# Performance work log

Measured on AMD Instinct MI355X. Metric: run time of the kernel, lower is better.

## Reference

```python
import jax, jax.numpy as jnp
import numpy as np

B, T, C = 1024, 512, 41


def setup_inputs() -> dict:
    key = jax.random.key(0)
    k1, k2, k3, k4 = jax.random.split(key, 4)
    x = jax.random.normal(k1, (B, T, C), dtype=jnp.float32)
    # torchcrf initializes all transition params uniform(-0.1, 0.1)
    start_transitions = jax.random.uniform(k2, (C,), minval=-0.1, maxval=0.1, dtype=jnp.float32)
    end_transitions = jax.random.uniform(k3, (C,), minval=-0.1, maxval=0.1, dtype=jnp.float32)
    transitions = jax.random.uniform(k4, (C, C), minval=-0.1, maxval=0.1, dtype=jnp.float32)
    return {"x": x, "start_transitions": start_transitions,
            "end_transitions": end_transitions, "transitions": transitions}


def reference(x, start_transitions, end_transitions, transitions):
    # Viterbi decode (torchcrf CRF.decode, batch_first, no mask -> full length)
    # x: [B, T, C] emissions
    score0 = start_transitions[None, :] + x[:, 0]  # [B, C]

    def step(score, emit_t):
        # score: [B, C] best score ending in each tag at time t
        # emit_t: [B, C] emissions at time t+1
        cand = score[:, :, None] + transitions[None, :, :] + emit_t[:, None, :]  # [B, Cprev, Cnext]
        best = jnp.max(cand, axis=1)      # [B, C]
        bp = jnp.argmax(cand, axis=1)     # [B, C] backpointer: best previous tag
        return best, bp

    emits = jnp.swapaxes(x[:, 1:], 0, 1)  # [T-1, B, C]
    final, bps = jax.lax.scan(step, score0, emits)
    final = final + end_transitions[None, :]  # [B, C]
    last_tag = jnp.argmax(final, axis=1)      # [B] tag at time T-1

    def back(tag, bp_t):
        # tag: [B] tag at time t+1; bp_t: [B, C] backpointers into time t
        prev = jnp.take_along_axis(bp_t, tag[:, None], axis=1)[:, 0]
        return prev, tag

    first_tag, tags_rest = jax.lax.scan(back, last_tag, bps, reverse=True)
    # tags_rest[t] is the tag at time t+1 (t = 0..T-2); first_tag is tag at time 0
    tags = jnp.concatenate([first_tag[:, None], jnp.swapaxes(tags_rest, 0, 1)], axis=1)  # [B, T]
    return tags.astype(jnp.int64)
```

## Files before the change

kernel.cpp:

```cpp
#include <hip/hip_runtime.h>

#define BB 1024
#define TT 512
#define CC 41
#define BPS 64

__device__ __forceinline__ float rlanef(float xv, int l) {
    return __int_as_float(__builtin_amdgcn_readlane(__float_as_int(xv), l));
}

__global__ __launch_bounds__(64) void crf_viterbi_kernel(
    const float* __restrict__ x,
    const float* __restrict__ start_t,
    const float* __restrict__ end_t,
    const float* __restrict__ trans,
    int* __restrict__ out)
{
    __shared__ unsigned char bp_lds[(TT - 1) * BPS];
    __shared__ int tags_lds[TT];

    const int lane = threadIdx.x;
    const int c = (lane < CC) ? lane : (CC - 1);

    float trans_reg[CC];
    #pragma unroll
    for (int p = 0; p < CC; ++p) trans_reg[p] = trans[p * CC + c];

    const float* xb = x + (size_t)blockIdx.x * TT * CC;

    float myscore = start_t[c] + xb[c];

    float emit_cur = xb[1 * CC + c];
    float emit_nxt = xb[2 * CC + c];

    for (int t = 1; t < TT; ++t) {
        const int tf = (t + 2 < TT) ? (t + 2) : (TT - 1);
        const float emit_fut = xb[(size_t)tf * CC + c];

        float sp[CC];
        #pragma unroll
        for (int p = 0; p < CC; ++p) sp[p] = rlanef(myscore, p);

        float v[CC];
        int  ix[CC];
        #pragma unroll
        for (int p = 0; p < CC; ++p) {
            v[p]  = (sp[p] + trans_reg[p]) + emit_cur;
            ix[p] = p;
        }

#define COMBINE(i, j) do { \
            if (v[(j)] > v[(i)]) { v[(i)] = v[(j)]; ix[(i)] = ix[(j)]; } \
        } while (0)
        #pragma unroll
        for (int i = 0; i < 20; ++i) COMBINE(2 * i, 2 * i + 1);
        #pragma unroll
        for (int i = 0; i < 10; ++i) COMBINE(4 * i, 4 * i + 2);
        #pragma unroll
        for (int i = 0; i < 5; ++i)  COMBINE(8 * i, 8 * i + 4);
        COMBINE(0, 8);
        COMBINE(16, 24);
        COMBINE(0, 16);
        COMBINE(32, 40);
        COMBINE(0, 32);
#undef COMBINE

        myscore = v[0];
        bp_lds[(t - 1) * BPS + lane] = (unsigned char)ix[0];

        emit_cur = emit_nxt;
        emit_nxt = emit_fut;
    }

    const float fin = myscore + end_t[c];

    float bestv = rlanef(fin, 0);
    int tag = 0;
    #pragma unroll
    for (int i = 1; i < CC; ++i) {
        const float vi = rlanef(fin, i);
        if (vi > bestv) { bestv = vi; tag = i; }
    }

    __syncthreads();

    if (lane == 0) tags_lds[TT - 1] = tag;
    for (int g = 31; g >= 0; --g) {
        const int base = g * 16;
        unsigned int rowv[16];
        #pragma unroll
        for (int j = 0; j < 16; ++j)
            rowv[j] = (unsigned int)bp_lds[(base + j) * BPS + lane];
        #pragma unroll
        for (int j = 15; j >= 0; --j) {
            const int r = base + j;
            if (r < TT - 1) {
                tag = (int)__builtin_amdgcn_readlane((int)rowv[j], tag);
                if (lane == 0) tags_lds[r] = tag;
            }
        }
    }
    __syncthreads();

    int* ob = out + (size_t)blockIdx.x * TT;
    #pragma unroll
    for (int i = 0; i < TT / 64; ++i) ob[lane + 64 * i] = tags_lds[lane + 64 * i];
}

extern "C" void kernel_launch(void* const* d_in, const int* in_sizes, int n_in,
                              void* d_out, int out_size, void* d_ws, size_t ws_size,
                              hipStream_t stream) {
    (void)in_sizes; (void)n_in; (void)d_ws; (void)ws_size; (void)out_size;
    const float* x       = (const float*)d_in[0];
    const float* start_t = (const float*)d_in[1];
    const float* end_t   = (const float*)d_in[2];
    const float* trans   = (const float*)d_in[3];
    int* out = (int*)d_out;

    crf_viterbi_kernel<<<dim3(BB), dim3(64), 0, stream>>>(x, start_t, end_t, trans, out);
}
```

Before: 266.4 us.

## Process two batch sequences per wavefront to interleave independent Viterbi chains

Each 64-lane block now decodes two batch rows at once, interleaving two independent max/argmax reduction trees and backtrace chains to expose instruction-level parallelism and hide readlane/LDS latency. The grid is halved, the backpointer row stride shrinks to 48 bytes, and emission prefetch is deepened to three steps. The trade-off is higher register pressure from duplicated v/ix arrays (launch_bounds min blocks set to 1) and fewer wavefronts in flight, which may cut occupancy on a 256-CU device.

```diff
diff --git a/kernel.cpp b/kernel.cpp
--- a/kernel.cpp
+++ b/kernel.cpp
@@ -3,21 +3,23 @@
 #define BB 1024
 #define TT 512
 #define CC 41
-#define BPS 64
+#define BPS 48
 
 __device__ __forceinline__ float rlanef(float xv, int l) {
     return __int_as_float(__builtin_amdgcn_readlane(__float_as_int(xv), l));
 }
 
-__global__ __launch_bounds__(64) void crf_viterbi_kernel(
+__global__ __launch_bounds__(64, 1) void crf_viterbi_kernel(
     const float* __restrict__ x,
     const float* __restrict__ start_t,
     const float* __restrict__ end_t,
     const float* __restrict__ trans,
     int* __restrict__ out)
 {
-    __shared__ unsigned char bp_lds[(TT - 1) * BPS];
-    __shared__ int tags_lds[TT];
+    __shared__ unsigned char bp0_lds[TT * BPS + 64];
+    __shared__ unsigned char bp1_lds[TT * BPS + 64];
+    __shared__ int tags0_lds[TT];
+    __shared__ int tags1_lds[TT];
 
     const int lane = threadIdx.x;
     const int c = (lane < CC) ? lane : (CC - 1);
@@ -26,85 +28,102 @@
     #pragma unroll
     for (int p = 0; p < CC; ++p) trans_reg[p] = trans[p * CC + c];
 
-    const float* xb = x + (size_t)blockIdx.x * TT * CC;
+    const int b0 = blockIdx.x * 2;
+    const int b1 = b0 + 1;
+    const float* xb0 = x + (size_t)b0 * TT * CC;
+    const float* xb1 = x + (size_t)b1 * TT * CC;
 
-    float myscore = start_t[c] + xb[c];
+    float sc0 = start_t[c] + xb0[c];
+    float sc1 = start_t[c] + xb1[c];
 
-    float emit_cur = xb[1 * CC + c];
-    float emit_nxt = xb[2 * CC + c];
+    float e0a = xb0[1 * CC + c], e0b = xb0[2 * CC + c], e0c = xb0[3 * CC + c];
+    float e1a = xb1[1 * CC + c], e1b = xb1[2 * CC + c], e1c = xb1[3 * CC + c];
 
     for (int t = 1; t < TT; ++t) {
-        const int tf = (t + 2 < TT) ? (t + 2) : (TT - 1);
-        const float emit_fut = xb[(size_t)tf * CC + c];
+        const int tf = (t + 3 < TT) ? (t + 3) : (TT - 1);
+        const float f0 = xb0[(size_t)tf * CC + c];
+        const float f1 = xb1[(size_t)tf * CC + c];
 
-        float sp[CC];
-        #pragma unroll
-        for (int p = 0; p < CC; ++p) sp[p] = rlanef(myscore, p);
-
-        float v[CC];
-        int  ix[CC];
+        float v0[CC], v1[CC];
+        int  ix0[CC], ix1[CC];
         #pragma unroll
         for (int p = 0; p < CC; ++p) {
-            v[p]  = (sp[p] + trans_reg[p]) + emit_cur;
-            ix[p] = p;
+            const float s0p = rlanef(sc0, p);
+            const float s1p = rlanef(sc1, p);
+            v0[p] = (s0p + trans_reg[p]) + e0a;  ix0[p] = p;
+            v1[p] = (s1p + trans_reg[p]) + e1a;  ix1[p] = p;
         }
 
-#define COMBINE(i, j) do { \
-            if (v[(j)] > v[(i)]) { v[(i)] = v[(j)]; ix[(i)] = ix[(j)]; } \
+#define CSTEP(V, IX, i, j) do { \
+            if (V[(j)] > V[(i)]) { V[(i)] = V[(j)]; IX[(i)] = IX[(j)]; } \
         } while (0)
         #pragma unroll
-        for (int i = 0; i < 20; ++i) COMBINE(2 * i, 2 * i + 1);
+        for (int i = 0; i < 20; ++i) { CSTEP(v0, ix0, 2*i, 2*i+1); CSTEP(v1, ix1, 2*i, 2*i+1); }
         #pragma unroll
-        for (int i = 0; i < 10; ++i) COMBINE(4 * i, 4 * i + 2);
+        for (int i = 0; i < 10; ++i) { CSTEP(v0, ix0, 4*i, 4*i+2); CSTEP(v1, ix1, 4*i, 4*i+2); }
         #pragma unroll
-        for (int i = 0; i < 5; ++i)  COMBINE(8 * i, 8 * i + 4);
-        COMBINE(0, 8);
-        COMBINE(16, 24);
-        COMBINE(0, 16);
-        COMBINE(32, 40);
-        COMBINE(0, 32);
-#undef COMBINE
+        for (int i = 0; i < 5;  ++i) { CSTEP(v0, ix0, 8*i, 8*i+4); CSTEP(v1, ix1, 8*i, 8*i+4); }
+        CSTEP(v0, ix0, 0, 8);   CSTEP(v1, ix1, 0, 8);
+        CSTEP(v0, ix0, 16, 24); CSTEP(v1, ix1, 16, 24);
+        CSTEP(v0, ix0, 0, 16);  CSTEP(v1, ix1, 0, 16);
+        CSTEP(v0, ix0, 32, 40); CSTEP(v1, ix1, 32, 40);
+        CSTEP(v0, ix0, 0, 32);  CSTEP(v1, ix1, 0, 32);
+#undef CSTEP
 
-        myscore = v[0];
-        bp_lds[(t - 1) * BPS + lane] = (unsigned char)ix[0];
+        sc0 = v0[0];
+        sc1 = v1[0];
+        if (lane < BPS) {
+            bp0_lds[(t - 1) * BPS + lane] = (unsigned char)ix0[0];
+            bp1_lds[(t - 1) * BPS + lane] = (unsigned char)ix1[0];
+        }
 
-        emit_cur = emit_nxt;
-        emit_nxt = emit_fut;
+        e0a = e0b; e0b = e0c; e0c = f0;
+        e1a = e1b; e1b = e1c; e1c = f1;
     }
 
-    const float fin = myscore + end_t[c];
+    const float fin0 = sc0 + end_t[c];
+    const float fin1 = sc1 + end_t[c];
 
-    float bestv = rlanef(fin, 0);
-    int tag = 0;
+    float bv0 = rlanef(fin0, 0); int tag0 = 0;
+    float bv1 = rlanef(fin1, 0); int tag1 = 0;
     #pragma unroll
     for (int i = 1; i < CC; ++i) {
-        const float vi = rlanef(fin, i);
-        if (vi > bestv) { bestv = vi; tag = i; }
+        const float q0 = rlanef(fin0, i);
+        const float q1 = rlanef(fin1, i);
+        if (q0 > bv0) { bv0 = q0; tag0 = i; }
+        if (q1 > bv1) { bv1 = q1; tag1 = i; }
     }
 
     __syncthreads();
 
-    if (lane == 0) tags_lds[TT - 1] = tag;
+    if (lane == 0) { tags0_lds[TT - 1] = tag0; tags1_lds[TT - 1] = tag1; }
     for (int g = 31; g >= 0; --g) {
         const int base = g * 16;
-        unsigned int rowv[16];
+        unsigned int r0[16], r1[16];
         #pragma unroll
-        for (int j = 0; j < 16; ++j)
-            rowv[j] = (unsigned int)bp_lds[(base + j) * BPS + lane];
+        for (int j = 0; j < 16; ++j) {
+            r0[j] = (unsigned int)bp0_lds[(base + j) * BPS + lane];
+            r1[j] = (unsigned int)bp1_lds[(base + j) * BPS + lane];
+        }
         #pragma unroll
         for (int j = 15; j >= 0; --j) {
             const int r = base + j;
             if (r < TT - 1) {
-                tag = (int)__builtin_amdgcn_readlane((int)rowv[j], tag);
-                if (lane == 0) tags_lds[r] = tag;
+                tag0 = (int)__builtin_amdgcn_readlane((int)r0[j], tag0);
+                tag1 = (int)__builtin_amdgcn_readlane((int)r1[j], tag1);
+                if (lane == 0) { tags0_lds[r] = tag0; tags1_lds[r] = tag1; }
             }
         }
     }
     __syncthreads();
 
-    int* ob = out + (size_t)blockIdx.x * TT;
+    int* ob0 = out + (size_t)b0 * TT;
+    int* ob1 = out + (size_t)b1 * TT;
     #pragma unroll
-    for (int i = 0; i < TT / 64; ++i) ob[lane + 64 * i] = tags_lds[lane + 64 * i];
+    for (int i = 0; i < TT / 64; ++i) {
+        ob0[lane + 64 * i] = tags0_lds[lane + 64 * i];
+        ob1[lane + 64 * i] = tags1_lds[lane + 64 * i];
+    }
 }
 
 extern "C" void kernel_launch(void* const* d_in, const int* in_sizes, int n_in,
@@ -117,5 +136,5 @@
     const float* trans   = (const float*)d_in[3];
     int* out = (int*)d_out;
 
-    crf_viterbi_kernel<<<dim3(BB), dim3(64), 0, stream>>>(x, start_t, end_t, trans, out);
+    crf_viterbi_kernel<<<dim3(BB / 2), dim3(64), 0, stream>>>(x, start_t, end_t, trans, out);
 }
```

New measurement: 723.6 us. 172% more time.
